# Kernel optimization log

Measured on AMD Instinct MI355X. Metric: run time of the kernel, lower is better.

Reference implementation:

```python
import jax, jax.numpy as jnp
import numpy as np

N, B, NPM = 16384, 256, 64          # nodes, molecules, nodes per molecule
E = 65536                           # edges
FMAX, AMAX = 32, 16                 # FG slots per molecule, atoms per FG
HID, FGE, POSE = 960, 512, 128
NFG, MAXTOK, NFEAT = 205, 160, 5


def setup_inputs() -> dict:
    key = jax.random.key(0)
    ks = jax.random.split(key, 12)
    graph_x = jax.random.normal(ks[0], (N, NFEAT), jnp.float32)
    edge_index = jax.random.randint(ks[1], (2, E), 0, N)
    graph_batch = jnp.arange(N) // NPM
    ptr = jnp.arange(B + 1) * NPM
    fg_type_tensor = jax.random.randint(ks[2], (B, FMAX), 0, NFG)
    idx = jax.random.randint(ks[3], (B, FMAX, AMAX), 0, NPM)
    drop = jax.random.uniform(ks[4], (B, FMAX, AMAX)) < 0.3
    fg_indices_tensor = jnp.where(drop, -1, idx)
    s = lambda k, sh: jax.random.normal(k, sh, jnp.float32) * 0.02
    return dict(
        graph_x=graph_x, edge_index=edge_index, graph_batch=graph_batch, ptr=ptr,
        fg_type_tensor=fg_type_tensor, fg_indices_tensor=fg_indices_tensor,
        W1=s(ks[5], (NFEAT, HID)), b1=jnp.zeros((HID,), jnp.float32),
        W2=s(ks[6], (HID, HID)), b2=jnp.zeros((HID,), jnp.float32),
        fg_embed=s(ks[7], (NFG, FGE)), pos_embed=s(ks[8], (MAXTOK, POSE)),
        projW=s(ks[9], (HID, HID)), projb=jnp.zeros((HID,), jnp.float32),
        fuseW=s(ks[10], (FGE + POSE + HID + HID, HID)), fuseb=jnp.zeros((HID,), jnp.float32),
    )


def gcn_conv(x, W, b, src, dst, n):
    # PyG GCNConv: linear, add self-loops, symmetric deg^-1/2 normalization, sum-aggregate, bias
    h = x @ W
    deg = 1.0 + jax.ops.segment_sum(jnp.ones(src.shape[0], h.dtype), dst, num_segments=n)
    dinv = jax.lax.rsqrt(deg)
    msg = h[src] * (dinv[src] * dinv[dst])[:, None]            # [E, HID]
    out = jax.ops.segment_sum(msg, dst, num_segments=n) + h * (dinv * dinv)[:, None]
    return out + b


def reference(graph_x, edge_index, graph_batch, ptr, fg_type_tensor, fg_indices_tensor,
              W1, b1, W2, b2, fg_embed, pos_embed, projW, projb, fuseW, fuseb):
    src, dst = edge_index[0], edge_index[1]
    n = graph_x.shape[0]
    h = jax.nn.relu(gcn_conv(graph_x, W1, b1, src, dst, n))
    h = gcn_conv(h, W2, b2, src, dst, n)

    Bsz, Fmax = fg_type_tensor.shape
    # global mean pool per molecule
    cnt = jax.ops.segment_sum(jnp.ones(n, h.dtype), graph_batch, num_segments=Bsz)
    global_emb = jax.ops.segment_sum(h, graph_batch, num_segments=Bsz) / cnt[:, None]

    fg_static = fg_embed[fg_type_tensor]                        # [B, F, FGE]
    fg_pos = jnp.broadcast_to(pos_embed[:Fmax][None], (Bsz, Fmax, pos_embed.shape[1]))

    # vectorized FG-specific node pooling (replaces nested python loops)
    mask = fg_indices_tensor >= 0                               # [B, F, A]
    gids = jnp.where(mask, ptr[:-1][:, None, None] + fg_indices_tensor, 0)
    gathered = h[gids] * mask[..., None].astype(h.dtype)        # [B, F, A, HID]
    counts = mask.sum(-1).astype(h.dtype)                       # [B, F]
    pooled = gathered.sum(-2) / jnp.maximum(counts, 1.0)[..., None]
    fg_valid_mask = counts > 0

    fg_node_proj = pooled @ projW + projb
    global_exp = jnp.broadcast_to(global_emb[:, None, :], (Bsz, Fmax, global_emb.shape[1]))
    fused = jnp.concatenate([fg_static, fg_pos, fg_node_proj, global_exp], axis=-1)
    fg_fused = fused @ fuseW + fuseb
    return fg_fused, fg_valid_mask
```

## Files before the change

kernel.cpp:

```cpp
#include <hip/hip_runtime.h>

typedef unsigned short u16;
typedef unsigned int u32;
typedef __attribute__((ext_vector_type(8))) short short8;
typedef __attribute__((ext_vector_type(4))) float f32x4;

#define N_NODES 16384
#define B_MOL   256
#define NPM     64
#define E_EDGES 65536
#define FMAXF   32
#define AMAXA   16
#define HID     960
#define NFG     205
#define BF_ROWS 8192
#define OUT1    7864320
#define NTOT    4516800

__device__ __forceinline__ float bf2f(u16 u){ u32 x=((u32)u)<<16; float f; __builtin_memcpy(&f,&x,4); return f; }
__device__ __forceinline__ u16 f2bf(float f){ u32 x; __builtin_memcpy(&x,&f,4); x += 0x7FFFu + ((x>>16)&1u); return (u16)(x>>16); }

__device__ __forceinline__ void gload_lds16(const u16* g, u16* l){
    __builtin_amdgcn_global_load_lds(
        (const __attribute__((address_space(1))) void*)g,
        (__attribute__((address_space(3))) void*)l, 16, 0, 0);
}
__device__ __forceinline__ size_t swzA(int row, int col){
    return ((size_t)((row>>4)*30 + (col>>5)))*512 + (size_t)(((((col>>3)&3)*16) + (row&15))*8);
}
__device__ __forceinline__ size_t swzE(int row, int col){
    return ((size_t)((row>>4)*30 + (col>>5)))*512 + (size_t)((((col>>3)&3)*16 + (row&15))*8 + (col&7));
}

struct NormSrcs { const void* p[11]; };
__global__ __launch_bounds__(256) void k_normAll(NormSrcs s, u16* __restrict__ region,
                                                 float* __restrict__ b2f, float* __restrict__ projbf,
                                                 float* __restrict__ z4, int* __restrict__ flag,
                                                 int* __restrict__ deg){
    __shared__ int cnt;
    int t = threadIdx.x;
    if (t==0) cnt = 0;
    __syncthreads();
    u16 pv = ((const u16*)s.p[0])[t*2];
    if (((pv>>7)&0xFF) >= 0xC0) atomicAdd(&cnt, 1);
    __syncthreads();
    int fl = (cnt > 16) ? 1 : 0;
    int i = blockIdx.x*256 + t;
    if (blockIdx.x==0 && t==0) *flag = fl;
    if (i < N_NODES) deg[i] = 0;
    if (i < 4*HID) z4[i] = 0.f;
    if (i >= NTOT) return;
    int seg, off;
    if      (i <   81920){seg=0;  off=i;}
    else if (i <   86720){seg=1;  off=i-81920;}
    else if (i <   87680){seg=2;  off=i-86720;}
    else if (i < 1009280){seg=3;  off=i-87680;}
    else if (i < 1010240){seg=4;  off=i-1009280;}
    else if (i < 1115200){seg=5;  off=i-1010240;}
    else if (i < 1135680){seg=6;  off=i-1115200;}
    else if (i < 2057280){seg=7;  off=i-1135680;}
    else if (i < 2058240){seg=8;  off=i-2057280;}
    else if (i < 4515840){seg=9;  off=i-2058240;}
    else                 {seg=10; off=i-4515840;}
    const void* sp = s.p[seg];
    float fv; u16 uv;
    if (fl){ fv = ((const float*)sp)[off]; uv = f2bf(fv); }
    else   { uv = ((const u16*)sp)[off];  fv = bf2f(uv); }
    region[i] = uv;
    if (seg==4) b2f[off] = fv;
    if (seg==8) projbf[off] = fv;
}


__device__ __forceinline__ void gemm_sq(int bx, int by, const u16* __restrict__ A, int lda,
                                        const u16* __restrict__ Bt, int ldb,
                                        u16* __restrict__ C, int swz, char* smem)
{
    u16* As = (u16*)smem;
    u16* Bs = (u16*)smem + 64*40;
    const int tid = threadIdx.x;
    const int wave = tid>>6, lane = tid&63;
    const int wm = wave>>1, wn = wave&1;
    const int q = lane>>4, l16 = lane&15;
    const int m0 = bx*64, n0 = by*64;
    const int sm = tid>>2, sk = (tid&3)*8;
    f32x4 acc00={0,0,0,0}, acc01={0,0,0,0}, acc10={0,0,0,0}, acc11={0,0,0,0};
    const u16* Ap = A + (size_t)(m0+sm)*lda + sk;
    const u16* Bp = Bt + (size_t)(n0+sm)*ldb + sk;
    for (int k0=0; k0<HID; k0+=32){
        short8 av = *(const short8*)(Ap + k0);
        short8 bv = *(const short8*)(Bp + k0);
        *(short8*)(As + sm*40 + sk) = av;
        *(short8*)(Bs + sm*40 + sk) = bv;
        __syncthreads();
        short8 a0 = *(const short8*)(As + (wm*32      + l16)*40 + q*8);
        short8 a1 = *(const short8*)(As + (wm*32 + 16 + l16)*40 + q*8);
        short8 b0 = *(const short8*)(Bs + (wn*32      + l16)*40 + q*8);
        short8 b1 = *(const short8*)(Bs + (wn*32 + 16 + l16)*40 + q*8);
        acc00 = __builtin_amdgcn_mfma_f32_16x16x32_bf16(a0,b0,acc00,0,0,0);
        acc01 = __builtin_amdgcn_mfma_f32_16x16x32_bf16(a0,b1,acc01,0,0,0);
        acc10 = __builtin_amdgcn_mfma_f32_16x16x32_bf16(a1,b0,acc10,0,0,0);
        acc11 = __builtin_amdgcn_mfma_f32_16x16x32_bf16(a1,b1,acc11,0,0,0);
        __syncthreads();
    }
    #pragma unroll
    for (int i=0;i<2;i++){
        int rowb = m0 + wm*32 + i*16 + q*4;
        #pragma unroll
        for (int j=0;j<2;j++){
            int col = n0 + wn*32 + j*16 + l16;
            f32x4 av = (i==0) ? ((j==0)?acc00:acc01) : ((j==0)?acc10:acc11);
            #pragma unroll
            for (int r=0;r<4;r++){
                int row = rowb + r;
                u16 o = f2bf(av[r]);
                if (swz) C[swzE(row,col)] = o;
                else     C[(size_t)row*HID + col] = o;
            }
        }
    }
}
__device__ __forceinline__ void gemm64f(int bx, int by, const u16* __restrict__ A, int lda,
                                        const u16* __restrict__ Bt, int ldb,
                                        float* __restrict__ C, int M, int K,
                                        const float* __restrict__ addv, char* smem)
{
    u16* As = (u16*)smem;
    u16* Bs = (u16*)smem + 64*40;
    const int tid = threadIdx.x;
    const int wave = tid>>6, lane = tid&63;
    const int wm = wave>>1, wn = wave&1;
    const int q = lane>>4, l16 = lane&15;
    const int m0 = bx*64, n0 = by*64;
    const int sm = tid>>2, sk = (tid&3)*8;
    f32x4 acc00={0,0,0,0}, acc01={0,0,0,0}, acc10={0,0,0,0}, acc11={0,0,0,0};
    const bool aOk = (m0+sm) < M;
    const u16* Ap = A + (size_t)(m0+sm)*lda + sk;
    const u16* Bp = Bt + (size_t)(n0+sm)*ldb + sk;
    for (int k0=0; k0<K; k0+=32){
        short8 av = {0,0,0,0,0,0,0,0};
        if (aOk) av = *(const short8*)(Ap + k0);
        short8 bv = *(const short8*)(Bp + k0);
        *(short8*)(As + sm*40 + sk) = av;
        *(short8*)(Bs + sm*40 + sk) = bv;
        __syncthreads();
        short8 a0 = *(const short8*)(As + (wm*32      + l16)*40 + q*8);
        short8 a1 = *(const short8*)(As + (wm*32 + 16 + l16)*40 + q*8);
        short8 b0 = *(const short8*)(Bs + (wn*32      + l16)*40 + q*8);
        short8 b1 = *(const short8*)(Bs + (wn*32 + 16 + l16)*40 + q*8);
        acc00 = __builtin_amdgcn_mfma_f32_16x16x32_bf16(a0,b0,acc00,0,0,0);
        acc01 = __builtin_amdgcn_mfma_f32_16x16x32_bf16(a0,b1,acc01,0,0,0);
        acc10 = __builtin_amdgcn_mfma_f32_16x16x32_bf16(a1,b0,acc10,0,0,0);
        acc11 = __builtin_amdgcn_mfma_f32_16x16x32_bf16(a1,b1,acc11,0,0,0);
        __syncthreads();
    }
    #pragma unroll
    for (int i=0;i<2;i++){
        int rowb = m0 + wm*32 + i*16 + q*4;
        #pragma unroll
        for (int j=0;j<2;j++){
            int col = n0 + wn*32 + j*16 + l16;
            f32x4 av = (i==0) ? ((j==0)?acc00:acc01) : ((j==0)?acc10:acc11);
            float add = addv ? addv[col] : 0.f;
            #pragma unroll
            for (int r=0;r<4;r++){
                int row = rowb + r;
                if (row < M) C[(size_t)row*HID + col] = av[r] + add;
            }
        }
    }
}
__device__ __forceinline__ void transpose_tile(int bx, int by, const u16* __restrict__ src,
                                               u16* __restrict__ dst, int R, int C, char* smem)
{
    u16 (*tl)[33] = (u16(*)[33])smem;
    int c0 = bx*32, r0 = by*32;
    int tx = threadIdx.x & 31, ty = threadIdx.x >> 5;
    #pragma unroll
    for (int i=0;i<4;i++) tl[ty+i*8][tx] = src[(size_t)(r0+ty+i*8)*C + c0+tx];
    __syncthreads();
    #pragma unroll
    for (int i=0;i<4;i++) dst[(size_t)(c0+ty+i*8)*R + r0+tx] = tl[tx][ty+i*8];
}
__device__ __forceinline__ void vecmat_body(int bx, int by, const float* __restrict__ v,
                                            const u16* __restrict__ M, float* __restrict__ out, char* smem)
{
    float (*part)[64] = (float(*)[64])smem;
    int tid = threadIdx.x;
    int cl = tid & 63;
    int c = bx*64 + cl;
    int kg = tid >> 6;
    int k0 = by*60 + kg*15;
    float s = 0.f;
    #pragma unroll
    for (int i=0;i<15;i++) s += v[k0+i]*bf2f(M[(size_t)(k0+i)*HID + c]);
    part[kg][cl] = s;
    __syncthreads();
    if (kg==0) atomicAdd(&out[c], part[0][cl]+part[1][cl]+part[2][cl]+part[3][cl]);
}
__device__ __forceinline__ void scandinv_body(const int* __restrict__ deg, int* __restrict__ off,
                                              int* __restrict__ cur, float* __restrict__ dinv, char* smem)
{
    int* ps = (int*)smem;
    int t = threadIdx.x;
    const int chunk = N_NODES/256;
    int base0 = t*chunk;
    int s = 0;
    for (int i=0;i<chunk;i++) s += deg[base0+i];
    ps[t] = s; __syncthreads();
    for (int ofs=1; ofs<256; ofs<<=1){
        int v = ps[t];
        int add = (t>=ofs) ? ps[t-ofs] : 0;
        __syncthreads();
        ps[t] = v + add;
        __syncthreads();
    }
    int run = (t==0) ? 0 : ps[t-1];
    for (int i=0;i<chunk;i++){
        int d = deg[base0+i];
        off[base0+i]=run; cur[base0+i]=run; run += d;
        dinv[base0+i] = rsqrtf(1.0f + (float)d);
    }
    if (t==255) off[N_NODES] = run;
}

__global__ __launch_bounds__(256) void k_L1(const u16* __restrict__ fuseWn, u16* __restrict__ fuseWT,
                                            const int* __restrict__ dst, int* __restrict__ deg){
    __shared__ __attribute__((aligned(16))) char smem[2112];
    int b = blockIdx.x;
    if (b < 2400){
        transpose_tile(b%30, b/30, fuseWn, fuseWT, 2560, HID, smem);
    } else {
        int e = (b-2400)*256 + threadIdx.x;
        if (e < E_EDGES) atomicAdd(&deg[dst[e]], 1);
    }
}
__global__ __launch_bounds__(256) void k_L2(const u16* fuseWT, const u16* projWn, const u16* W2n,
                                            u16* Ub, u16* WglobT,
                                            const int* deg, int* off, int* cur, float* dinv){
    __shared__ __attribute__((aligned(16))) char smem[10240];
    int b = blockIdx.x;
    if (b < 450){
        int z = b/225, r = b%225;
        if (z==0) gemm_sq(r%15, r/15, fuseWT+640, 2560, projWn, HID, Ub, 0, smem);
        else      gemm_sq(r%15, r/15, fuseWT+1600, 2560, W2n, HID, WglobT, 0, smem);
    } else {
        scandinv_body(deg, off, cur, dinv, smem);
    }
}
__global__ __launch_bounds__(256) void k_L3(const u16* Ub, const u16* W2n, u16* WbigS,
                                            const u16* fgeN, const u16* posN, const u16* fuseWT,
                                            float* fgA, float* pWbM,
                                            const int* src, const int* dst, const float* dinv,
                                            int* cur, int* csr_s, float* csr_w){
    __shared__ __attribute__((aligned(16))) char smem[10240];
    int b = blockIdx.x;
    if (b < 225){
        gemm_sq(b%15, b/15, Ub, HID, W2n, HID, WbigS, 1, smem);
    } else if (b < 300){
        int bb = b-225;
        if (bb < 60) gemm64f(bb%4, bb/4, fgeN, 512, fuseWT, 2560, fgA, NFG, 512, nullptr, smem);
        else         gemm64f(0, bb-60, posN, 128, fuseWT+512, 2560, pWbM, FMAXF, 128, nullptr, smem);
    } else {
        int e = (b-300)*256 + threadIdx.x;
        if (e < E_EDGES){
            int s = src[e], d = dst[e];
            int p = atomicAdd(&cur[d], 1);
            csr_s[p] = s;
            csr_w[p] = dinv[s]*dinv[d];
        }
    }
}
__global__ __launch_bounds__(256) void k_L4(const u16* __restrict__ gxn, const float* __restrict__ dinv,
                                            const int* __restrict__ off, const int* __restrict__ csr_s,
                                            const float* __restrict__ csr_w,
                                            const u16* __restrict__ W1, const u16* __restrict__ b1,
                                            u16* __restrict__ h1b,
                                            const float* b2f, const float* projbf, const u16* fuseWn,
                                            const u16* projWn, float* tvb, float* cC, float* gvec){
    __shared__ __attribute__((aligned(16))) char smem[1024];
    int b = blockIdx.x;
    if (b < 8192){
        float* a2 = (float*)smem;
        int t = threadIdx.x;
        int h = t>>7, tl = t&127;
        int n = b*2 + h;
        if (tl < 5){
            int k = tl;
            float di = dinv[n], sw = di*di;
            float a = sw * bf2f(gxn[n*5+k]);
            int j0 = off[n], j1 = off[n+1];
            for (int j=j0;j<j1;j++) a += csr_w[j]*bf2f(gxn[csr_s[j]*5+k]);
            a2[h*8+k] = a;
        }
        __syncthreads();
        if (tl < 120){
            int c8 = tl*8;
            float a[5];
            #pragma unroll
            for (int k=0;k<5;k++) a[k] = a2[h*8+k];
            float r[8];
            short8 bb = *(const short8*)(b1 + c8);
            #pragma unroll
            for (int j=0;j<8;j++) r[j] = bf2f(((u16*)&bb)[j]);
            #pragma unroll
            for (int k=0;k<5;k++){
                short8 wv = *(const short8*)(W1 + k*HID + c8);
                #pragma unroll
                for (int j=0;j<8;j++) r[j] += a[k]*bf2f(((u16*)&wv)[j]);
            }
            short8 o;
            #pragma unroll
            for (int j=0;j<8;j++) ((u16*)&o)[j] = f2bf(fmaxf(r[j],0.f));
            *(short8*)(h1b + (size_t)n*HID + c8) = o;
        }
    } else {
        int bb = b - 8192;
        int z = bb/240, r = bb%240;
        if (z==0)      vecmat_body(r%15, r/15, b2f,    projWn,            tvb,  smem);
        else if (z==1) vecmat_body(r%15, r/15, projbf, fuseWn + 640*HID,  cC,   smem);
        else           vecmat_body(r%15, r/15, b2f,    fuseWn + 1600*HID, gvec, smem);
    }
}
__global__ __launch_bounds__(256) void k_L5(const u16* __restrict__ h1b, const float* __restrict__ dinv,
                                            const int* __restrict__ off, const int* __restrict__ csr_s,
                                            const float* __restrict__ csr_w, u16* __restrict__ P1b,
                                            const float* tvb, const u16* fuseWn, float* vb,
                                            const float* cC, const float* gvec, const u16* fusebn, float* c0){
    __shared__ __attribute__((aligned(16))) char smem[1024];
    int b = blockIdx.x;
    if (b < 4096){
        int wv = threadIdx.x>>6, lane = threadIdx.x&63;
        int n = b*4 + wv;
        int c = lane*16;
        bool act = lane < 60;
        float di = dinv[n], sw = di*di;
        float acc[16];
        if (act){
            short8 h0 = *(const short8*)(h1b + (size_t)n*HID + c);
            short8 h1v = *(const short8*)(h1b + (size_t)n*HID + c + 8);
            #pragma unroll
            for (int j=0;j<8;j++){ acc[j] = sw*bf2f(((u16*)&h0)[j]); acc[8+j] = sw*bf2f(((u16*)&h1v)[j]); }
        } else {
            #pragma unroll
            for (int j=0;j<16;j++) acc[j] = 0.f;
        }
        int j0 = off[n], j1 = off[n+1];
        for (int j=j0;j<j1;j++){
            int s = csr_s[j]; float w = csr_w[j];
            if (act){
                short8 v0 = *(const short8*)(h1b + (size_t)s*HID + c);
                short8 v1 = *(const short8*)(h1b + (size_t)s*HID + c + 8);
                #pragma unroll
                for (int j2=0;j2<8;j2++){ acc[j2] += w*bf2f(((u16*)&v0)[j2]); acc[8+j2] += w*bf2f(((u16*)&v1)[j2]); }
            }
        }
        if (act){
            short8 o0, o1;
            #pragma unroll
            for (int j=0;j<8;j++){ ((u16*)&o0)[j] = f2bf(acc[j]); ((u16*)&o1)[j] = f2bf(acc[8+j]); }
            *(short8*)(P1b + (size_t)n*HID + c) = o0;
            *(short8*)(P1b + (size_t)n*HID + c + 8) = o1;
        }
    } else if (b < 4336){
        int bb = b - 4096;
        vecmat_body(bb%15, bb/15, tvb, fuseWn + 640*HID, vb, smem);
    } else {
        int c = (b-4336)*256 + threadIdx.x;
        if (c < HID) c0[c] = cC[c] + gvec[c] + bf2f(fusebn[c]);
    }
}
__global__ __launch_bounds__(256) void k_L6(const u16* __restrict__ P1b, const int* __restrict__ fgi,
                                            const int* __restrict__ ptr, u16* __restrict__ prb,
                                            float* __restrict__ evec, u16* __restrict__ maskb,
                                            float* __restrict__ maskf, const int* __restrict__ flag,
                                            u16* __restrict__ gmb){
    int b = blockIdx.x;
    if (b < 2048){
        int wv = threadIdx.x>>6, lane = threadIdx.x&63;
        int bf = b*4 + wv;
        int mb = bf >> 5;
        int base = ptr[mb];
        int c = lane*16;
        bool act = lane < 60;
        float acc[16];
        #pragma unroll
        for (int j=0;j<16;j++) acc[j] = 0.f;
        int cnt = 0;
        #pragma unroll
        for (int a=0;a<AMAXA;a++){
            int idx = fgi[bf*AMAXA + a];
            if (idx >= 0){
                cnt++;
                if (act){
                    short8 v0 = *(const short8*)(P1b + (size_t)(base+idx)*HID + c);
                    short8 v1 = *(const short8*)(P1b + (size_t)(base+idx)*HID + c + 8);
                    #pragma unroll
                    for (int j=0;j<8;j++){ acc[j] += bf2f(((u16*)&v0)[j]); acc[8+j] += bf2f(((u16*)&v1)[j]); }
                }
            }
        }
        float inv = (cnt>0) ? 1.0f/(float)cnt : 0.0f;
        if (act){
            short8 o0, o1;
            #pragma unroll
            for (int j=0;j<8;j++){ ((u16*)&o0)[j] = f2bf(acc[j]*inv); ((u16*)&o1)[j] = f2bf(acc[8+j]*inv); }
            *(short8*)(prb + swzA(bf, c)) = o0;
            *(short8*)(prb + swzA(bf, c+8)) = o1;
        }
        if (lane == 0){
            float e = (cnt>0) ? 1.0f : 0.0f;
            evec[bf] = e;
            if (*flag) maskf[bf] = e;
            else       maskb[bf] = f2bf(e);
        }
    } else {
        int id = (b-2048)*256 + threadIdx.x;
        int mb = id / 120; int c8 = (id - mb*120)*8;
        float s[8] = {0,0,0,0,0,0,0,0};
        for (int i=0;i<NPM;i++){
            short8 v = *(const short8*)(P1b + (size_t)(mb*NPM+i)*HID + c8);
            #pragma unroll
            for (int j=0;j<8;j++) s[j] += bf2f(((u16*)&v)[j]);
        }
        const float inv = 1.0f/(float)NPM;
        short8 o;
        #pragma unroll
        for (int j=0;j<8;j++) ((u16*)&o)[j] = f2bf(s[j]*inv);
        *(short8*)(gmb + (size_t)mb*HID + c8) = o;
    }
}
__global__ __launch_bounds__(256) void k_L7(const u16* gmb, const u16* WglobT, float* Gc, const float* c0){
    __shared__ __attribute__((aligned(16))) char smem[10240];
    int b = blockIdx.x;
    gemm64f(b%4, b/4, gmb, HID, WglobT, HID, Gc, B_MOL, HID, c0, smem);
}

__global__ __launch_bounds__(256) void k_gemmF(
    const u16* __restrict__ A, const u16* __restrict__ Bt,
    float* __restrict__ Cf, u16* __restrict__ Cb,
    const int* __restrict__ fg_type, const float* __restrict__ evec,
    const float* __restrict__ fgA, const float* __restrict__ pWbM,
    const float* __restrict__ vb, const float* __restrict__ Gc,
    const int* __restrict__ flag)
{
    __shared__ __attribute__((aligned(16))) u16 S[2][14*512];
    const int tid = threadIdx.x;
    const int wave = tid>>6, lane = tid&63;
    const int wm = wave>>1, wn = wave&1;
    const int q = lane>>4, l16 = lane&15;
    const int m0 = blockIdx.x*128, n0 = blockIdx.y*96;
    const int R0 = blockIdx.x*8, N0 = blockIdx.y*6;

    f32x4 acc[4][3];
    #pragma unroll
    for (int i=0;i<4;i++)
        #pragma unroll
        for (int j=0;j<3;j++) acc[i][j] = (f32x4){0,0,0,0};

    const u16* gA0 = A  + ((size_t)(R0 + wave*2    )*30)*512 + lane*8;
    const u16* gA1 = A  + ((size_t)(R0 + wave*2 + 1)*30)*512 + lane*8;
    const u16* gB0 = Bt + ((size_t)(N0 + wave      )*30)*512 + lane*8;
    const u16* gB1 = Bt + ((size_t)(N0 + 4 + wave  )*30)*512 + lane*8;

    gload_lds16(gA0, &S[0][(wave*2  )*512]);
    gload_lds16(gA1, &S[0][(wave*2+1)*512]);
    gload_lds16(gB0, &S[0][(8+wave)*512]);
    if (wave < 2) gload_lds16(gB1, &S[0][(12+wave)*512]);

    int buf = 0;
    for (int kc=0; kc<30; kc++){
        __syncthreads();
        if (kc < 29){
            int kn = (kc+1)*512;
            gload_lds16(gA0 + kn, &S[buf^1][(wave*2  )*512]);
            gload_lds16(gA1 + kn, &S[buf^1][(wave*2+1)*512]);
            gload_lds16(gB0 + kn, &S[buf^1][(8+wave)*512]);
            if (wave < 2) gload_lds16(gB1 + kn, &S[buf^1][(12+wave)*512]);
        }
        short8 af[4], bfr[3];
        #pragma unroll
        for (int i=0;i<4;i++) af[i] = *(const short8*)(&S[buf][(wm*4+i)*512 + lane*8]);
        #pragma unroll
        for (int j=0;j<3;j++) bfr[j] = *(const short8*)(&S[buf][(8+wn*3+j)*512 + lane*8]);
        #pragma unroll
        for (int i=0;i<4;i++)
            #pragma unroll
            for (int j=0;j<3;j++)
                acc[i][j] = __builtin_amdgcn_mfma_f32_16x16x32_bf16(af[i], bfr[j], acc[i][j], 0,0,0);
        buf ^= 1;
    }

    const int isf = *flag;
    #pragma unroll
    for (int i=0;i<4;i++){
        int rowb = m0 + wm*64 + i*16 + q*4;
        #pragma unroll
        for (int r=0;r<4;r++){
            int row = rowb + r;
            int bb = row>>5, ff = row&31;
            int ty = fg_type[row];
            float e = evec[row];
            #pragma unroll
            for (int j=0;j<3;j++){
                int col = n0 + wn*48 + j*16 + l16;
                float v = acc[i][j][r]
                        + fgA[ty*HID+col] + pWbM[ff*HID+col]
                        + e*vb[col] + Gc[bb*HID+col];
                if (isf) Cf[(size_t)row*HID + col] = v;
                else     Cb[(size_t)row*HID + col] = f2bf(v);
            }
        }
    }
}

extern "C" void kernel_launch(void* const* d_in, const int* in_sizes, int n_in,
                              void* d_out, int out_size, void* d_ws, size_t ws_size,
                              hipStream_t stream) {
    const int* edge_idx  = (const int*)d_in[1];
    const int* ptr       = (const int*)d_in[3];
    const int* fg_type   = (const int*)d_in[4];
    const int* fg_idx    = (const int*)d_in[5];

    char* w = (char*)d_ws;
    auto nxt = [&](size_t b)->char*{ char* p = w; w += (b + 255) & ~(size_t)255; return p; };
    u16* big0   = (u16*)nxt((size_t)N_NODES*HID*2);
    u16* fuseWT = big0;
    u16* Ub     = big0 + (size_t)HID*2560;
    u16* h1b    = big0;
    u16* prb    = big0;
    u16* P1b    = (u16*)nxt((size_t)N_NODES*HID*2);
    u16*  WbigS  = (u16*) nxt((size_t)HID*HID*2);
    u16*  WglobT = (u16*) nxt((size_t)HID*HID*2);
    float* fgA   = (float*)nxt((size_t)NFG*HID*4);
    float* pWbM  = (float*)nxt((size_t)FMAXF*HID*4);
    float* b2f   = (float*)nxt(HID*4);
    float* projbf= (float*)nxt(HID*4);
    float* tvb   = (float*)nxt(HID*4);
    float* cC    = (float*)nxt(HID*4);
    float* gvec  = (float*)nxt(HID*4);
    float* vb    = (float*)nxt(HID*4);
    float* c0    = (float*)nxt(HID*4);
    int*   deg   = (int*)  nxt(N_NODES*4);
    float* dinv  = (float*)nxt(N_NODES*4);
    int*   off   = (int*)  nxt((N_NODES+1)*4);
    int*   cur   = (int*)  nxt(N_NODES*4);
    int*   csr_s = (int*)  nxt(E_EDGES*4);
    float* csr_w = (float*)nxt(E_EDGES*4);
    float* evec  = (float*)nxt(BF_ROWS*4);
    u16*   gmb   = (u16*)  nxt((size_t)B_MOL*HID*2);
    float* Gc    = (float*)nxt((size_t)B_MOL*HID*4);
    int*   flag  = (int*)  nxt(256);
    u16*   region= (u16*)  nxt((size_t)NTOT*2);
    u16* gxn    = region;
    u16* W1n    = region +   81920;
    u16* b1n    = region +   86720;
    u16* W2n    = region +   87680;
    u16* fgeN   = region + 1010240;
    u16* posN   = region + 1115200;
    u16* projWn = region + 1135680;
    u16* fuseWn = region + 2058240;
    u16* fusebn = region + 4515840;

    NormSrcs ns;
    ns.p[0]=d_in[0]; ns.p[1]=d_in[6]; ns.p[2]=d_in[7]; ns.p[3]=d_in[8]; ns.p[4]=d_in[9];
    ns.p[5]=d_in[10]; ns.p[6]=d_in[11]; ns.p[7]=d_in[12]; ns.p[8]=d_in[13]; ns.p[9]=d_in[14]; ns.p[10]=d_in[15];
    k_normAll<<<(NTOT+255)/256,256,0,stream>>>(ns, region, b2f, projbf, tvb, flag, deg);
    k_L1<<<2656,256,0,stream>>>(fuseWn, fuseWT, edge_idx + E_EDGES, deg);
    k_L2<<<451,256,0,stream>>>(fuseWT, projWn, W2n, Ub, WglobT, deg, off, cur, dinv);
    k_L3<<<556,256,0,stream>>>(Ub, W2n, WbigS, fgeN, posN, fuseWT, fgA, pWbM,
                               edge_idx, edge_idx + E_EDGES, dinv, cur, csr_s, csr_w);
    k_L4<<<8912,256,0,stream>>>(gxn, dinv, off, csr_s, csr_w, W1n, b1n, h1b,
                                b2f, projbf, fuseWn, projWn, tvb, cC, gvec);
    k_L5<<<4340,256,0,stream>>>(h1b, dinv, off, csr_s, csr_w, P1b,
                                tvb, fuseWn, vb, cC, gvec, fusebn, c0);
    k_L6<<<2168,256,0,stream>>>(P1b, fg_idx, ptr, prb, evec,
                                (u16*)d_out + OUT1, (float*)d_out + OUT1, flag, gmb);
    k_L7<<<60,256,0,stream>>>(gmb, WglobT, Gc, c0);
    k_gemmF<<<dim3(64,10),256,0,stream>>>(prb, WbigS, (float*)d_out, (u16*)d_out,
                                          fg_type, evec, fgA, pWbM, vb, Gc, flag);
    (void)in_sizes; (void)n_in; (void)out_size; (void)ws_size;
}
```

Measured before the change: 290.9 us.

## Triple-buffer gemmF K-loop with fine-grained vmcnt waits and MFMA priority

Replaces the double-buffered LDS pipeline in the fused output GEMM with a three-stage ring, prefetching two K-chunks ahead. It uses explicit s_waitcnt vmcnt counts plus a raw s_barrier instead of __syncthreads, so each wave waits only for the oldest chunk's loads. It also raises wave priority around the MFMA block. This costs 50% more LDS per block, which may reduce occupancy, and depends on the hand-counted vmcnt values being correct.

Result: no change. 291.5 us (+0.2%).

```diff
diff --git a/kernel.cpp b/kernel.cpp
--- a/kernel.cpp
+++ b/kernel.cpp
@@ -444,7 +444,7 @@
     const float* __restrict__ vb, const float* __restrict__ Gc,
     const int* __restrict__ flag)
 {
-    __shared__ __attribute__((aligned(16))) u16 S[2][14*512];
+    __shared__ __attribute__((aligned(16))) u16 S[3][14*512];
     const int tid = threadIdx.x;
     const int wave = tid>>6, lane = tid&63;
     const int wm = wave>>1, wn = wave&1;
@@ -463,32 +463,55 @@
     const u16* gB0 = Bt + ((size_t)(N0 + wave      )*30)*512 + lane*8;
     const u16* gB1 = Bt + ((size_t)(N0 + 4 + wave  )*30)*512 + lane*8;
 
-    gload_lds16(gA0, &S[0][(wave*2  )*512]);
-    gload_lds16(gA1, &S[0][(wave*2+1)*512]);
-    gload_lds16(gB0, &S[0][(8+wave)*512]);
-    if (wave < 2) gload_lds16(gB1, &S[0][(12+wave)*512]);
-
-    int buf = 0;
+    u16* sA = &S[0][0];
+    u16* sB = &S[1][0];
+    u16* sC = &S[2][0];
+
+    {
+        gload_lds16(gA0, sA + (wave*2  )*512);
+        gload_lds16(gA1, sA + (wave*2+1)*512);
+        gload_lds16(gB0, sA + (8+wave)*512);
+        if (wave < 2) gload_lds16(gB1, sA + (12+wave)*512);
+        const int kn = 512;
+        gload_lds16(gA0 + kn, sB + (wave*2  )*512);
+        gload_lds16(gA1 + kn, sB + (wave*2+1)*512);
+        gload_lds16(gB0 + kn, sB + (8+wave)*512);
+        if (wave < 2) gload_lds16(gB1 + kn, sB + (12+wave)*512);
+    }
+    if (wave < 2) asm volatile("s_waitcnt vmcnt(4)" ::: "memory");
+    else          asm volatile("s_waitcnt vmcnt(3)" ::: "memory");
+    __builtin_amdgcn_s_barrier();
+
     for (int kc=0; kc<30; kc++){
-        __syncthreads();
-        if (kc < 29){
-            int kn = (kc+1)*512;
-            gload_lds16(gA0 + kn, &S[buf^1][(wave*2  )*512]);
-            gload_lds16(gA1 + kn, &S[buf^1][(wave*2+1)*512]);
-            gload_lds16(gB0 + kn, &S[buf^1][(8+wave)*512]);
-            if (wave < 2) gload_lds16(gB1 + kn, &S[buf^1][(12+wave)*512]);
+        if (kc+2 < 30){
+            const int kn = (kc+2)*512;
+            gload_lds16(gA0 + kn, sC + (wave*2  )*512);
+            gload_lds16(gA1 + kn, sC + (wave*2+1)*512);
+            gload_lds16(gB0 + kn, sC + (8+wave)*512);
+            if (wave < 2) gload_lds16(gB1 + kn, sC + (12+wave)*512);
         }
         short8 af[4], bfr[3];
         #pragma unroll
-        for (int i=0;i<4;i++) af[i] = *(const short8*)(&S[buf][(wm*4+i)*512 + lane*8]);
-        #pragma unroll
-        for (int j=0;j<3;j++) bfr[j] = *(const short8*)(&S[buf][(8+wn*3+j)*512 + lane*8]);
+        for (int i=0;i<4;i++) af[i] = *(const short8*)(sA + (wm*4+i)*512 + lane*8);
+        #pragma unroll
+        for (int j=0;j<3;j++) bfr[j] = *(const short8*)(sA + (8+wn*3+j)*512 + lane*8);
+        __builtin_amdgcn_s_setprio(1);
         #pragma unroll
         for (int i=0;i<4;i++)
             #pragma unroll
             for (int j=0;j<3;j++)
                 acc[i][j] = __builtin_amdgcn_mfma_f32_16x16x32_bf16(af[i], bfr[j], acc[i][j], 0,0,0);
-        buf ^= 1;
+        __builtin_amdgcn_s_setprio(0);
+        if (kc < 29){
+            if (kc < 28){
+                if (wave < 2) asm volatile("s_waitcnt vmcnt(4)" ::: "memory");
+                else          asm volatile("s_waitcnt vmcnt(3)" ::: "memory");
+            } else {
+                asm volatile("s_waitcnt vmcnt(0)" ::: "memory");
+            }
+            __builtin_amdgcn_s_barrier();
+        }
+        u16* t = sA; sA = sB; sB = sC; sC = t;
     }
 
     const int isf = *flag;
```
